# Performance work log

Measured on AMD Instinct MI355X. Metric: run time of the kernel, lower is better.

The kernel has to match this reference:

```python
import jax, jax.numpy as jnp
import numpy as np

N_Q = 8
DIM = 128
CODEBOOK_SIZE = 1024


def setup_inputs() -> dict:
    key = jax.random.key(0)
    k1, k2 = jax.random.split(key)
    x = jax.random.normal(k1, (8, DIM, 4096), dtype=jnp.float32)
    codebooks = jax.random.normal(k2, (N_Q, CODEBOOK_SIZE, DIM), dtype=jnp.float32)
    return {"x": x, "codebooks": codebooks, "frame_rate": 75}


def _rvq(xt, codebooks):
    # xt: (B, T, D); codebooks: (n_q, K, D)
    def stage(carry, cb):
        residual, qout = carry
        # squared euclidean distance (B, T, K); argmin == Encodec's argmax of -dist
        d = (jnp.sum(residual * residual, axis=-1, keepdims=True)
             - 2.0 * jnp.einsum('btd,kd->btk', residual, cb)
             + jnp.sum(cb * cb, axis=-1))
        idx = jnp.argmin(d, axis=-1)                     # (B, T)
        q = cb[idx]                                       # gather: (B, T, D)
        # commit loss: mse(quantize.detach(), input)
        commit = jnp.mean((jax.lax.stop_gradient(q) - residual) ** 2)
        # straight-through estimator
        q_st = residual + jax.lax.stop_gradient(q - residual)
        return (residual - q_st, qout + q_st), (idx, commit)

    init = (xt, jnp.zeros_like(xt))
    (_, qout), (codes, commits) = jax.lax.scan(stage, init, codebooks)
    return qout, codes, commits


def reference(x, codebooks, frame_rate):
    # x: (B, D, T) -> (B, T, D)
    xt = jnp.swapaxes(x, 1, 2)
    qout, codes, commits = _rvq(xt, codebooks)
    quantized = jnp.swapaxes(qout, 1, 2)                 # (B, D, T)
    n_q, K, _ = codebooks.shape
    bw_per_q = np.log2(K) * frame_rate
    bw = jnp.asarray(n_q * bw_per_q, dtype=jnp.float32)
    penalty = jnp.mean(commits)
    return quantized, codes, bw, penalty
```

## Files before the change

kernel.cpp:

```cpp
#include <hip/hip_runtime.h>
#include <math.h>

#define Bsz 8
#define Dd  128
#define Tt  4096
#define Kk  1024
#define NQ  8
#define BT  (Bsz*Tt)
#define MT  128
#define NTHR 512
#define WV  8
#define DELTA 0.05f

typedef float f32x4 __attribute__((ext_vector_type(4)));
typedef short short8 __attribute__((ext_vector_type(8)));

__device__ __forceinline__ unsigned short f2bf(float x) {
    unsigned u = __float_as_uint(x);
    u += 0x7FFF + ((u >> 16) & 1);
    return (unsigned short)(u >> 16);
}
__device__ __forceinline__ float bf2f(unsigned short h) {
    return __uint_as_float(((unsigned)h) << 16);
}

__global__ void k_init(const float* __restrict__ x,
                       float* __restrict__ resid) {
    __shared__ float tile[32][33];
    int b  = blockIdx.z;
    int t0 = blockIdx.x * 32, d0 = blockIdx.y * 32;
    int tx = threadIdx.x, ty = threadIdx.y;
    #pragma unroll
    for (int k = 0; k < 4; k++) {
        int d = d0 + ty + k * 8;
        tile[ty + k * 8][tx] = x[((size_t)(b * Dd + d)) * Tt + t0 + tx];
    }
    __syncthreads();
    #pragma unroll
    for (int k = 0; k < 4; k++) {
        int t = t0 + ty + k * 8;
        resid[((size_t)(b * Tt + t)) * Dd + d0 + tx] = tile[tx][ty + k * 8];
    }
}

__global__ void k_prep(const float* __restrict__ cb, char* __restrict__ bswz) {
    int ln = threadIdx.x;
    int kc = blockIdx.x & 3;
    int t  = (blockIdx.x >> 2) & 63;
    int q  = blockIdx.x >> 8;
    int code = t * 16 + (ln & 15);
    int d0   = kc * 32 + (ln >> 4) * 8;
    const float* src = cb + ((size_t)(q * Kk + code)) * Dd + d0;
    float v[8];
    *(float4*)&v[0] = *(const float4*)src;
    *(float4*)&v[4] = *(const float4*)(src + 4);
    short8 h, l;
    #pragma unroll
    for (int j = 0; j < 8; j++) {
        unsigned short hu = f2bf(v[j]);
        h[j] = (short)hu;
        l[j] = (short)f2bf(v[j] - bf2f(hu));
    }
    char* base = bswz + ((size_t)(q * 64 + t)) * 8192;
    *(short8*)(base + kc * 1024 + ln * 16) = h;
    *(short8*)(base + 4096 + kc * 1024 + ln * 16) = l;
}

__global__ void k_c2(const float* __restrict__ cb,
                     float* __restrict__ c2,
                     double* __restrict__ commits) {
    int row  = blockIdx.x * 4 + (threadIdx.x >> 6);
    int lane = threadIdx.x & 63;
    const float* p = cb + (size_t)row * Dd;
    float a = p[lane], b = p[lane + 64];
    float s = a * a + b * b;
    #pragma unroll
    for (int off = 32; off; off >>= 1) s += __shfl_down(s, off);
    if (lane == 0) c2[row] = s;
    if (blockIdx.x == 0 && threadIdx.x < NQ) commits[threadIdx.x] = 0.0;
}

__device__ __forceinline__ float exact_score(const float* __restrict__ rrow,
                                             const float* __restrict__ crow,
                                             float c2v) {
    float a = 0.0f;
    #pragma unroll
    for (int d4 = 0; d4 < 32; d4++) {
        float4 r = *(const float4*)(rrow + d4 * 4);
        float4 c = *(const float4*)(crow + d4 * 4);
        a = fmaf(r.x, c.x, a); a = fmaf(r.y, c.y, a);
        a = fmaf(r.z, c.z, a); a = fmaf(r.w, c.w, a);
    }
    return fmaf(-2.0f, a, c2v);
}

__global__ __launch_bounds__(NTHR, 2) void k_rvq_fused(
        float* __restrict__ resid,
        const float* __restrict__ cb,
        const char*  __restrict__ bswz,
        const float* __restrict__ c2g,
        float* __restrict__ codes_f,
        double* __restrict__ commits) {
    __shared__ float rlds[MT][Dd];
    __shared__ float c2s[Kk];
    __shared__ f32x4 bbuf[2][NTHR];
    __shared__ float fb1[MT], fb2[MT], fb3[MT];
    __shared__ int   fi1[MT], fi2[MT];
    __shared__ int   sidxs[MT];
    __shared__ int   nfall, flist[MT];
    __shared__ float fwv[WV]; __shared__ int fwi[WV];
    __shared__ float csum[WV];

    const int tid  = threadIdx.x;
    const int w    = tid >> 6, ln = tid & 63;
    const int quad = ln >> 4,  m  = ln & 15;
    const int base = blockIdx.x * MT;
    const int prow = w * 16 + m;

    {
        const f32x4* src = (const f32x4*)(resid + (size_t)base * Dd);
        f32x4* dst = (f32x4*)&rlds[0][0];
        #pragma unroll
        for (int i = 0; i < (MT * Dd / 4) / NTHR; i++)
            dst[tid + i * NTHR] = src[tid + i * NTHR];
    }
    bbuf[0][tid] = *((const f32x4*)bswz + tid);
    int par = 0;
    __syncthreads();

    #pragma unroll 1
    for (int q = 0; q < NQ; q++) {
        const float* cbq = cb + (size_t)q * Kk * Dd;
        #pragma unroll
        for (int i = 0; i < Kk / NTHR; i++)
            c2s[tid + i * NTHR] = c2g[q * Kk + tid + i * NTHR];
        if (tid == 0) nfall = 0;

        short8 Ah[4], Al[4];
        #pragma unroll
        for (int kc = 0; kc < 4; kc++) {
            const float* rp = &rlds[prow][kc * 32 + quad * 8];
            float v[8];
            *(f32x4*)&v[0] = *(const f32x4*)rp;
            *(f32x4*)&v[4] = *(const f32x4*)(rp + 4);
            short8 h, l;
            #pragma unroll
            for (int j = 0; j < 8; j++) {
                unsigned short hu = f2bf(v[j]);
                h[j] = (short)hu;
                l[j] = (short)f2bf(v[j] - bf2f(hu));
            }
            Ah[kc] = h; Al[kc] = l;
        }

        float b1[4], b2[4], b3[4]; int i1[4], i2[4];
        #pragma unroll
        for (int j = 0; j < 4; j++) {
            b1[j] = INFINITY; b2[j] = INFINITY; b3[j] = INFINITY;
            i1[j] = 0; i2[j] = 0;
        }
        __syncthreads();

        #pragma unroll 2
        for (int t = 0; t < 64; t++) {
            const int tt = q * 64 + t;
            const bool havestg = (tt + 1 < NQ * 64);
            f32x4 stg;
            if (havestg)
                stg = *((const f32x4*)(bswz + (size_t)(tt + 1) * 8192) + tid);

            const char* bb = (const char*)&bbuf[par][0];
            f32x4 acc01 = {0.f, 0.f, 0.f, 0.f};
            f32x4 acc23 = {0.f, 0.f, 0.f, 0.f};
            #pragma unroll
            for (int kc = 0; kc < 4; kc++) {
                short8 ch = *(const short8*)(bb + kc * 1024 + ln * 16);
                short8 cl = *(const short8*)(bb + 4096 + kc * 1024 + ln * 16);
                if (kc < 2) {
                    acc01 = __builtin_amdgcn_mfma_f32_16x16x32_bf16(Al[kc], ch, acc01, 0, 0, 0);
                    acc01 = __builtin_amdgcn_mfma_f32_16x16x32_bf16(Ah[kc], cl, acc01, 0, 0, 0);
                    acc01 = __builtin_amdgcn_mfma_f32_16x16x32_bf16(Ah[kc], ch, acc01, 0, 0, 0);
                } else {
                    acc23 = __builtin_amdgcn_mfma_f32_16x16x32_bf16(Al[kc], ch, acc23, 0, 0, 0);
                    acc23 = __builtin_amdgcn_mfma_f32_16x16x32_bf16(Ah[kc], cl, acc23, 0, 0, 0);
                    acc23 = __builtin_amdgcn_mfma_f32_16x16x32_bf16(Ah[kc], ch, acc23, 0, 0, 0);
                }
            }
            float c2v  = c2s[t * 16 + m];
            int   code = t * 16 + m;
            #pragma unroll
            for (int j = 0; j < 4; j++) {
                float s = fmaf(-2.0f, acc01[j] + acc23[j], c2v);
                bool lt1 = s < b1[j];
                bool lt2 = s < b2[j];
                b3[j] = __builtin_amdgcn_fmed3f(s, b2[j], b3[j]);
                b2[j] = __builtin_amdgcn_fmed3f(s, b1[j], b2[j]);
                i2[j] = lt1 ? i1[j] : (lt2 ? code : i2[j]);
                i1[j] = lt1 ? code : i1[j];
                b1[j] = fminf(b1[j], s);
            }
            if (havestg) bbuf[par ^ 1][tid] = stg;
            __syncthreads();
            par ^= 1;
        }

        #pragma unroll
        for (int j = 0; j < 4; j++) {
            float v1 = b1[j], v2 = b2[j], v3 = b3[j];
            int   a1 = i1[j], a2 = i2[j];
            #pragma unroll
            for (int off = 1; off < 16; off <<= 1) {
                float w1 = __shfl_xor(v1, off); int j1 = __shfl_xor(a1, off);
                float w2 = __shfl_xor(v2, off); int j2 = __shfl_xor(a2, off);
                float w3 = __shfl_xor(v3, off);
                bool aw = (v1 < w1) || (v1 == w1 && a1 < j1);
                float x1 = aw ? v1 : w1, x2 = aw ? v2 : w2, x3 = aw ? v3 : w3;
                int   y1 = aw ? a1 : j1, y2 = aw ? a2 : j2;
                float z1 = aw ? w1 : v1, z2 = aw ? w2 : v2;
                int   u1 = aw ? j1 : a1;
                bool s2a = (x2 < z1) || (x2 == z1 && y2 < u1);
                v1 = x1; a1 = y1;
                v2 = s2a ? x2 : z1; a2 = s2a ? y2 : u1;
                v3 = s2a ? fminf(x3, z1) : fminf(x2, z2);
            }
            if (m == 0) {
                int p = w * 16 + quad * 4 + j;
                fb1[p] = v1; fb2[p] = v2; fb3[p] = v3;
                fi1[p] = a1; fi2[p] = a2;
            }
        }
        __syncthreads();

        if (tid < MT) {
            int p = tid;
            float v1 = fb1[p], v2 = fb2[p], v3 = fb3[p];
            int   a1 = fi1[p], a2 = fi2[p];
            if (v3 <= v1 + DELTA) {
                int sl = atomicAdd(&nfall, 1);
                flist[sl] = p;
            } else {
                int bk = a1;
                if (v2 <= v1 + DELTA) {
                    const float* rrow = &rlds[p][0];
                    float s1 = exact_score(rrow, cbq + (size_t)a1 * Dd, c2s[a1]);
                    float s2 = exact_score(rrow, cbq + (size_t)a2 * Dd, c2s[a2]);
                    if (s2 < s1 || (s2 == s1 && a2 < a1)) bk = a2;
                }
                sidxs[p] = bk;
                codes_f[(size_t)q * BT + base + p] = (float)bk;
            }
        }
        __syncthreads();

        for (int fi = 0; fi < nfall; fi++) {
            int p = flist[fi];
            const float* rrow = &rlds[p][0];
            float bv = INFINITY; int bk = 0;
            #pragma unroll
            for (int c = 0; c < 2; c++) {
                int k = tid * 2 + c;
                float sc = exact_score(rrow, cbq + (size_t)k * Dd, c2s[k]);
                if (sc < bv || (sc == bv && k < bk)) { bv = sc; bk = k; }
            }
            #pragma unroll
            for (int off = 32; off; off >>= 1) {
                float v2 = __shfl_xor(bv, off);
                int   k2 = __shfl_xor(bk, off);
                if (v2 < bv || (v2 == bv && k2 < bk)) { bv = v2; bk = k2; }
            }
            if (ln == 0) { fwv[w] = bv; fwi[w] = bk; }
            __syncthreads();
            if (tid == 0) {
                float v = fwv[0]; int k = fwi[0];
                #pragma unroll
                for (int w2 = 1; w2 < WV; w2++) {
                    if (fwv[w2] < v || (fwv[w2] == v && fwi[w2] < k)) {
                        v = fwv[w2]; k = fwi[w2];
                    }
                }
                sidxs[p] = k;
                codes_f[(size_t)q * BT + base + p] = (float)k;
            }
            __syncthreads();
        }
        __syncthreads();

        {
            const int idx = sidxs[prow];
            const float* qrow = cbq + (size_t)idx * Dd;
            float cacc = 0.0f;
            #pragma unroll
            for (int kc = 0; kc < 4; kc++) {
                const int d0 = kc * 32 + quad * 8;
                float r[8], qv[8], nr[8];
                *(f32x4*)&r[0]  = *(const f32x4*)&rlds[prow][d0];
                *(f32x4*)&r[4]  = *(const f32x4*)&rlds[prow][d0 + 4];
                *(f32x4*)&qv[0] = *(const f32x4*)(qrow + d0);
                *(f32x4*)&qv[4] = *(const f32x4*)(qrow + d0 + 4);
                #pragma unroll
                for (int j = 0; j < 8; j++) {
                    float t1 = qv[j] - r[j];
                    float qs = r[j] + t1;
                    nr[j] = r[j] - qs;
                    cacc = fmaf(t1, t1, cacc);
                }
                *(f32x4*)&rlds[prow][d0]     = *(f32x4*)&nr[0];
                *(f32x4*)&rlds[prow][d0 + 4] = *(f32x4*)&nr[4];
            }
            #pragma unroll
            for (int off = 32; off; off >>= 1) cacc += __shfl_down(cacc, off);
            if (ln == 0) csum[w] = cacc;
        }
        __syncthreads();
        if (tid == 0) {
            double sd = 0.0;
            #pragma unroll
            for (int w2 = 0; w2 < WV; w2++) sd += (double)csum[w2];
            atomicAdd(commits + q, sd);
        }
        __syncthreads();
    }

    {
        f32x4* dst = (f32x4*)(resid + (size_t)base * Dd);
        const f32x4* src = (const f32x4*)&rlds[0][0];
        #pragma unroll
        for (int i = 0; i < (MT * Dd / 4) / NTHR; i++)
            dst[tid + i * NTHR] = src[tid + i * NTHR];
    }
}

__global__ void k_final(const float* __restrict__ x,
                        const float* __restrict__ resid,
                        float* __restrict__ outq) {
    __shared__ float tile[32][33];
    int b  = blockIdx.z;
    int t0 = blockIdx.x * 32, d0 = blockIdx.y * 32;
    int tx = threadIdx.x, ty = threadIdx.y;
    #pragma unroll
    for (int k = 0; k < 4; k++) {
        int t = t0 + ty + k * 8;
        tile[ty + k * 8][tx] = resid[((size_t)(b * Tt + t)) * Dd + d0 + tx];
    }
    __syncthreads();
    #pragma unroll
    for (int k = 0; k < 4; k++) {
        int d = d0 + ty + k * 8;
        size_t o = ((size_t)(b * Dd + d)) * Tt + t0 + tx;
        outq[o] = x[o] - tile[tx][ty + k * 8];
    }
}

__global__ void k_scalars(const double* __restrict__ commits,
                          const int* __restrict__ frame_rate,
                          float* __restrict__ outs) {
    if (threadIdx.x == 0 && blockIdx.x == 0) {
        double s = 0.0;
        #pragma unroll
        for (int q = 0; q < NQ; q++) s += commits[q];
        double per_elem = s / ((double)NQ * (double)BT * (double)Dd);
        outs[0] = (float)(NQ * 10.0 * (double)frame_rate[0]);
        outs[1] = (float)per_elem;
    }
}

extern "C" void kernel_launch(void* const* d_in, const int* in_sizes, int n_in,
                              void* d_out, int out_size, void* d_ws, size_t ws_size,
                              hipStream_t stream) {
    const float* x  = (const float*)d_in[0];
    const float* cb = (const float*)d_in[1];
    const int*   fr = (const int*)d_in[2];

    float* outq    = (float*)d_out;
    float* codes_f = outq + (size_t)Bsz * Dd * Tt;
    float* scal    = codes_f + (size_t)NQ * BT;

    char* ws = (char*)d_ws;
    float*  resid   = (float*)ws;
    float*  c2      = resid + (size_t)BT * Dd;
    double* commits = (double*)(c2 + (size_t)NQ * Kk);
    char*   bswz    = (char*)(commits + NQ);

    dim3 tb(32, 8, 1);
    k_init<<<dim3(Tt / 32, Dd / 32, Bsz), tb, 0, stream>>>(x, resid);
    k_prep<<<NQ * 256, 64, 0, stream>>>(cb, bswz);
    k_c2<<<NQ * Kk / 4, 256, 0, stream>>>(cb, c2, commits);

    k_rvq_fused<<<BT / MT, NTHR, 0, stream>>>(resid, cb, bswz, c2,
                                              codes_f, commits);

    k_final<<<dim3(Tt / 32, Dd / 32, Bsz), tb, 0, stream>>>(x, resid, outq);
    k_scalars<<<1, 64, 0, stream>>>(commits, fr, scal);
}
```

Baseline: 507.6 us.

## Split codebook across wave halves, two row tiles per wave, async LDS loads

Each wave now holds two 16-row A fragments and processes half of the codebook tiles, so every B fragment read from LDS feeds twice as many MFMAs. The two halves' top-3 candidates are merged afterwards. Codebook tiles are streamed straight into LDS with global_load_lds using explicit waitcnt and barriers in place of register staging. The residual tile in LDS is XOR-swizzled to avoid bank conflicts, and MFMA sections run at raised priority. The cost is more registers per thread (which may limit occupancy at 2 blocks per CU), an extra merge step, and more complex synchronisation.

```diff
diff --git a/kernel.cpp b/kernel.cpp
--- a/kernel.cpp
+++ b/kernel.cpp
@@ -22,6 +22,12 @@
 }
 __device__ __forceinline__ float bf2f(unsigned short h) {
     return __uint_as_float(((unsigned)h) << 16);
+}
+
+__device__ __forceinline__ void gload_lds16(const void* g, void* l) {
+    __builtin_amdgcn_global_load_lds(
+        (const __attribute__((address_space(1))) unsigned int*)g,
+        (__attribute__((address_space(3))) unsigned int*)l, 16, 0, 0);
 }
 
 __global__ void k_init(const float* __restrict__ x,
@@ -80,16 +86,20 @@
     if (blockIdx.x == 0 && threadIdx.x < NQ) commits[threadIdx.x] = 0.0;
 }
 
-__device__ __forceinline__ float exact_score(const float* __restrict__ rrow,
-                                             const float* __restrict__ crow,
-                                             float c2v) {
+__device__ __forceinline__ float exact_score_sw(const float* __restrict__ rldsb,
+                                                int p,
+                                                const float* __restrict__ crow,
+                                                float c2v) {
+    const f32x4* r4 = (const f32x4*)rldsb;
+    const f32x4* c4 = (const f32x4*)crow;
+    int rb = p * 32, sw = p & 7;
     float a = 0.0f;
     #pragma unroll
     for (int d4 = 0; d4 < 32; d4++) {
-        float4 r = *(const float4*)(rrow + d4 * 4);
-        float4 c = *(const float4*)(crow + d4 * 4);
-        a = fmaf(r.x, c.x, a); a = fmaf(r.y, c.y, a);
-        a = fmaf(r.z, c.z, a); a = fmaf(r.w, c.w, a);
+        f32x4 r = r4[rb + (d4 ^ sw)];
+        f32x4 c = c4[d4];
+        a = fmaf(r[0], c[0], a); a = fmaf(r[1], c[1], a);
+        a = fmaf(r[2], c[2], a); a = fmaf(r[3], c[3], a);
     }
     return fmaf(-2.0f, a, c2v);
 }
@@ -101,11 +111,12 @@
         const float* __restrict__ c2g,
         float* __restrict__ codes_f,
         double* __restrict__ commits) {
-    __shared__ float rlds[MT][Dd];
+    __shared__ float rlds[MT * Dd];
     __shared__ float c2s[Kk];
-    __shared__ f32x4 bbuf[2][NTHR];
-    __shared__ float fb1[MT], fb2[MT], fb3[MT];
-    __shared__ int   fi1[MT], fi2[MT];
+    __shared__ f32x4 bbuf[2][2][512];
+    __shared__ float fA1[MT], fA2[MT], fA3[MT];
+    __shared__ float fB1[MT], fB2[MT], fB3[MT];
+    __shared__ int   iA1[MT], iA2[MT], iB1[MT], iB2[MT];
     __shared__ int   sidxs[MT];
     __shared__ int   nfall, flist[MT];
     __shared__ float fwv[WV]; __shared__ int fwi[WV];
@@ -114,136 +125,201 @@
     const int tid  = threadIdx.x;
     const int w    = tid >> 6, ln = tid & 63;
     const int quad = ln >> 4,  m  = ln & 15;
+    const int wg   = w & 3,    half = w >> 2;
+    const int toff = half * 32;
     const int base = blockIdx.x * MT;
-    const int prow = w * 16 + m;
+    const int prow0 = wg * 32 + m;
+    const int prow1 = wg * 32 + 16 + m;
+
+    f32x4* r4 = (f32x4*)rlds;
 
     {
         const f32x4* src = (const f32x4*)(resid + (size_t)base * Dd);
-        f32x4* dst = (f32x4*)&rlds[0][0];
-        #pragma unroll
-        for (int i = 0; i < (MT * Dd / 4) / NTHR; i++)
-            dst[tid + i * NTHR] = src[tid + i * NTHR];
-    }
-    bbuf[0][tid] = *((const f32x4*)bswz + tid);
-    int par = 0;
+        #pragma unroll
+        for (int i = 0; i < (MT * Dd / 4) / NTHR; i++) {
+            int idx = tid + i * NTHR;
+            int row = idx >> 5, c4 = idx & 31;
+            r4[row * 32 + (c4 ^ (row & 7))] = src[idx];
+        }
+    }
     __syncthreads();
 
     #pragma unroll 1
     for (int q = 0; q < NQ; q++) {
         const float* cbq = cb + (size_t)q * Kk * Dd;
+        const char*  bsq = bswz + (size_t)q * 64 * 8192;
         #pragma unroll
         for (int i = 0; i < Kk / NTHR; i++)
             c2s[tid + i * NTHR] = c2g[q * Kk + tid + i * NTHR];
         if (tid == 0) nfall = 0;
 
-        short8 Ah[4], Al[4];
+        short8 Ah0[4], Al0[4], Ah1[4], Al1[4];
         #pragma unroll
         for (int kc = 0; kc < 4; kc++) {
-            const float* rp = &rlds[prow][kc * 32 + quad * 8];
+            int c4a = kc * 8 + quad * 2;
             float v[8];
-            *(f32x4*)&v[0] = *(const f32x4*)rp;
-            *(f32x4*)&v[4] = *(const f32x4*)(rp + 4);
             short8 h, l;
+            *(f32x4*)&v[0] = r4[prow0 * 32 + (c4a ^ (prow0 & 7))];
+            *(f32x4*)&v[4] = r4[prow0 * 32 + ((c4a + 1) ^ (prow0 & 7))];
             #pragma unroll
             for (int j = 0; j < 8; j++) {
                 unsigned short hu = f2bf(v[j]);
                 h[j] = (short)hu;
                 l[j] = (short)f2bf(v[j] - bf2f(hu));
             }
-            Ah[kc] = h; Al[kc] = l;
-        }
-
-        float b1[4], b2[4], b3[4]; int i1[4], i2[4];
+            Ah0[kc] = h; Al0[kc] = l;
+            *(f32x4*)&v[0] = r4[prow1 * 32 + (c4a ^ (prow1 & 7))];
+            *(f32x4*)&v[4] = r4[prow1 * 32 + ((c4a + 1) ^ (prow1 & 7))];
+            #pragma unroll
+            for (int j = 0; j < 8; j++) {
+                unsigned short hu = f2bf(v[j]);
+                h[j] = (short)hu;
+                l[j] = (short)f2bf(v[j] - bf2f(hu));
+            }
+            Ah1[kc] = h; Al1[kc] = l;
+        }
+
+        float b1a[4], b2a[4], b3a[4], b1b[4], b2b[4], b3b[4];
+        int   i1a[4], i2a[4], i1b[4], i2b[4];
         #pragma unroll
         for (int j = 0; j < 4; j++) {
-            b1[j] = INFINITY; b2[j] = INFINITY; b3[j] = INFINITY;
-            i1[j] = 0; i2[j] = 0;
-        }
-        __syncthreads();
-
-        #pragma unroll 2
-        for (int t = 0; t < 64; t++) {
-            const int tt = q * 64 + t;
-            const bool havestg = (tt + 1 < NQ * 64);
-            f32x4 stg;
-            if (havestg)
-                stg = *((const f32x4*)(bswz + (size_t)(tt + 1) * 8192) + tid);
-
-            const char* bb = (const char*)&bbuf[par][0];
-            f32x4 acc01 = {0.f, 0.f, 0.f, 0.f};
-            f32x4 acc23 = {0.f, 0.f, 0.f, 0.f};
+            b1a[j] = INFINITY; b2a[j] = INFINITY; b3a[j] = INFINITY;
+            b1b[j] = INFINITY; b2b[j] = INFINITY; b3b[j] = INFINITY;
+            i1a[j] = 0; i2a[j] = 0; i1b[j] = 0; i2b[j] = 0;
+        }
+        __syncthreads();
+
+        gload_lds16(bsq + (size_t)toff * 0 + 0 * 8192 + w * 1024 + ln * 16,
+                    (char*)&bbuf[0][0][0] + w * 1024);
+        gload_lds16(bsq + (size_t)32 * 8192 + w * 1024 + ln * 16,
+                    (char*)&bbuf[0][1][0] + w * 1024);
+        int par = 0;
+
+        #pragma unroll 1
+        for (int s = 0; s < 32; s++) {
+            asm volatile("s_waitcnt vmcnt(0)" ::: "memory");
+            __builtin_amdgcn_s_barrier();
+            __builtin_amdgcn_sched_barrier(0);
+            if (s + 1 < 32) {
+                gload_lds16(bsq + (size_t)(s + 1) * 8192 + w * 1024 + ln * 16,
+                            (char*)&bbuf[par ^ 1][0][0] + w * 1024);
+                gload_lds16(bsq + (size_t)(32 + s + 1) * 8192 + w * 1024 + ln * 16,
+                            (char*)&bbuf[par ^ 1][1][0] + w * 1024);
+            }
+            const char* bb = (const char*)&bbuf[par][half][0];
+            f32x4 a01a = {0.f,0.f,0.f,0.f}, a23a = {0.f,0.f,0.f,0.f};
+            f32x4 a01b = {0.f,0.f,0.f,0.f}, a23b = {0.f,0.f,0.f,0.f};
+            __builtin_amdgcn_s_setprio(1);
             #pragma unroll
             for (int kc = 0; kc < 4; kc++) {
                 short8 ch = *(const short8*)(bb + kc * 1024 + ln * 16);
                 short8 cl = *(const short8*)(bb + 4096 + kc * 1024 + ln * 16);
                 if (kc < 2) {
-                    acc01 = __builtin_amdgcn_mfma_f32_16x16x32_bf16(Al[kc], ch, acc01, 0, 0, 0);
-                    acc01 = __builtin_amdgcn_mfma_f32_16x16x32_bf16(Ah[kc], cl, acc01, 0, 0, 0);
-                    acc01 = __builtin_amdgcn_mfma_f32_16x16x32_bf16(Ah[kc], ch, acc01, 0, 0, 0);
+                    a01a = __builtin_amdgcn_mfma_f32_16x16x32_bf16(Al0[kc], ch, a01a, 0, 0, 0);
+                    a01a = __builtin_amdgcn_mfma_f32_16x16x32_bf16(Ah0[kc], cl, a01a, 0, 0, 0);
+                    a01a = __builtin_amdgcn_mfma_f32_16x16x32_bf16(Ah0[kc], ch, a01a, 0, 0, 0);
+                    a01b = __builtin_amdgcn_mfma_f32_16x16x32_bf16(Al1[kc], ch, a01b, 0, 0, 0);
+                    a01b = __builtin_amdgcn_mfma_f32_16x16x32_bf16(Ah1[kc], cl, a01b, 0, 0, 0);
+                    a01b = __builtin_amdgcn_mfma_f32_16x16x32_bf16(Ah1[kc], ch, a01b, 0, 0, 0);
                 } else {
-                    acc23 = __builtin_amdgcn_mfma_f32_16x16x32_bf16(Al[kc], ch, acc23, 0, 0, 0);
-                    acc23 = __builtin_amdgcn_mfma_f32_16x16x32_bf16(Ah[kc], cl, acc23, 0, 0, 0);
-                    acc23 = __builtin_amdgcn_mfma_f32_16x16x32_bf16(Ah[kc], ch, acc23, 0, 0, 0);
+                    a23a = __builtin_amdgcn_mfma_f32_16x16x32_bf16(Al0[kc], ch, a23a, 0, 0, 0);
+                    a23a = __builtin_amdgcn_mfma_f32_16x16x32_bf16(Ah0[kc], cl, a23a, 0, 0, 0);
+                    a23a = __builtin_amdgcn_mfma_f32_16x16x32_bf16(Ah0[kc], ch, a23a, 0, 0, 0);
+                    a23b = __builtin_amdgcn_mfma_f32_16x16x32_bf16(Al1[kc], ch, a23b, 0, 0, 0);
+                    a23b = __builtin_amdgcn_mfma_f32_16x16x32_bf16(Ah1[kc], cl, a23b, 0, 0, 0);
+                    a23b = __builtin_amdgcn_mfma_f32_16x16x32_bf16(Ah1[kc], ch, a23b, 0, 0, 0);
                 }
             }
-            float c2v  = c2s[t * 16 + m];
-            int   code = t * 16 + m;
+            __builtin_amdgcn_s_setprio(0);
+            float c2v  = c2s[(toff + s) * 16 + m];
+            int   code = (toff + s) * 16 + m;
             #pragma unroll
             for (int j = 0; j < 4; j++) {
-                float s = fmaf(-2.0f, acc01[j] + acc23[j], c2v);
-                bool lt1 = s < b1[j];
-                bool lt2 = s < b2[j];
-                b3[j] = __builtin_amdgcn_fmed3f(s, b2[j], b3[j]);
-                b2[j] = __builtin_amdgcn_fmed3f(s, b1[j], b2[j]);
-                i2[j] = lt1 ? i1[j] : (lt2 ? code : i2[j]);
-                i1[j] = lt1 ? code : i1[j];
-                b1[j] = fminf(b1[j], s);
-            }
-            if (havestg) bbuf[par ^ 1][tid] = stg;
-            __syncthreads();
+                float sc = fmaf(-2.0f, a01a[j] + a23a[j], c2v);
+                bool lt1 = sc < b1a[j];
+                bool lt2 = sc < b2a[j];
+                b3a[j] = __builtin_amdgcn_fmed3f(sc, b2a[j], b3a[j]);
+                b2a[j] = __builtin_amdgcn_fmed3f(sc, b1a[j], b2a[j]);
+                i2a[j] = lt1 ? i1a[j] : (lt2 ? code : i2a[j]);
+                i1a[j] = lt1 ? code : i1a[j];
+                b1a[j] = fminf(b1a[j], sc);
+                float sd = fmaf(-2.0f, a01b[j] + a23b[j], c2v);
+                bool mt1 = sd < b1b[j];
+                bool mt2 = sd < b2b[j];
+                b3b[j] = __builtin_amdgcn_fmed3f(sd, b2b[j], b3b[j]);
+                b2b[j] = __builtin_amdgcn_fmed3f(sd, b1b[j], b2b[j]);
+                i2b[j] = mt1 ? i1b[j] : (mt2 ? code : i2b[j]);
+                i1b[j] = mt1 ? code : i1b[j];
+                b1b[j] = fminf(b1b[j], sd);
+            }
+            asm volatile("s_waitcnt lgkmcnt(0)" ::: "memory");
+            __builtin_amdgcn_sched_barrier(0);
             par ^= 1;
         }
 
         #pragma unroll
-        for (int j = 0; j < 4; j++) {
-            float v1 = b1[j], v2 = b2[j], v3 = b3[j];
-            int   a1 = i1[j], a2 = i2[j];
-            #pragma unroll
-            for (int off = 1; off < 16; off <<= 1) {
-                float w1 = __shfl_xor(v1, off); int j1 = __shfl_xor(a1, off);
-                float w2 = __shfl_xor(v2, off); int j2 = __shfl_xor(a2, off);
-                float w3 = __shfl_xor(v3, off);
-                bool aw = (v1 < w1) || (v1 == w1 && a1 < j1);
-                float x1 = aw ? v1 : w1, x2 = aw ? v2 : w2, x3 = aw ? v3 : w3;
-                int   y1 = aw ? a1 : j1, y2 = aw ? a2 : j2;
-                float z1 = aw ? w1 : v1, z2 = aw ? w2 : v2;
-                int   u1 = aw ? j1 : a1;
-                bool s2a = (x2 < z1) || (x2 == z1 && y2 < u1);
-                v1 = x1; a1 = y1;
-                v2 = s2a ? x2 : z1; a2 = s2a ? y2 : u1;
-                v3 = s2a ? fminf(x3, z1) : fminf(x2, z2);
-            }
-            if (m == 0) {
-                int p = w * 16 + quad * 4 + j;
-                fb1[p] = v1; fb2[p] = v2; fb3[p] = v3;
-                fi1[p] = a1; fi2[p] = a2;
+        for (int set = 0; set < 2; set++) {
+            #pragma unroll
+            for (int j = 0; j < 4; j++) {
+                float v1 = set ? b1b[j] : b1a[j];
+                float v2 = set ? b2b[j] : b2a[j];
+                float v3 = set ? b3b[j] : b3a[j];
+                int   a1 = set ? i1b[j] : i1a[j];
+                int   a2 = set ? i2b[j] : i2a[j];
+                #pragma unroll
+                for (int off = 1; off < 16; off <<= 1) {
+                    float w1 = __shfl_xor(v1, off); int j1 = __shfl_xor(a1, off);
+                    float w2 = __shfl_xor(v2, off); int j2 = __shfl_xor(a2, off);
+                    float w3 = __shfl_xor(v3, off);
+                    bool aw = (v1 < w1) || (v1 == w1 && a1 < j1);
+                    float x1 = aw ? v1 : w1, x2 = aw ? v2 : w2, x3 = aw ? v3 : w3;
+                    int   y1 = aw ? a1 : j1, y2 = aw ? a2 : j2;
+                    float z1 = aw ? w1 : v1, z2 = aw ? w2 : v2;
+                    int   u1 = aw ? j1 : a1;
+                    bool s2a = (x2 < z1) || (x2 == z1 && y2 < u1);
+                    v1 = x1; a1 = y1;
+                    v2 = s2a ? x2 : z1; a2 = s2a ? y2 : u1;
+                    v3 = s2a ? fminf(x3, z1) : fminf(x2, z2);
+                }
+                if (m == 0) {
+                    int p = wg * 32 + set * 16 + quad * 4 + j;
+                    if (half == 0) {
+                        fA1[p] = v1; fA2[p] = v2; fA3[p] = v3;
+                        iA1[p] = a1; iA2[p] = a2;
+                    } else {
+                        fB1[p] = v1; fB2[p] = v2; fB3[p] = v3;
+                        iB1[p] = a1; iB2[p] = a2;
+                    }
+                }
             }
         }
         __syncthreads();
 
         if (tid < MT) {
             int p = tid;
-            float v1 = fb1[p], v2 = fb2[p], v3 = fb3[p];
-            int   a1 = fi1[p], a2 = fi2[p];
+            float vA1 = fA1[p], vA2 = fA2[p], vA3 = fA3[p];
+            int   aA1 = iA1[p], aA2 = iA2[p];
+            float vB1 = fB1[p], vB2 = fB2[p], vB3 = fB3[p];
+            int   aB1 = iB1[p], aB2 = iB2[p];
+            bool aw = (vA1 < vB1) || (vA1 == vB1 && aA1 < aB1);
+            float x1 = aw ? vA1 : vB1, x2 = aw ? vA2 : vB2, x3 = aw ? vA3 : vB3;
+            int   y1 = aw ? aA1 : aB1, y2 = aw ? aA2 : aB2;
+            float z1 = aw ? vB1 : vA1, z2 = aw ? vB2 : vA2;
+            int   u1 = aw ? aB1 : aA1;
+            bool s2a = (x2 < z1) || (x2 == z1 && y2 < u1);
+            float v1 = x1;
+            float v2 = s2a ? x2 : z1;
+            float v3 = s2a ? fminf(x3, z1) : fminf(x2, z2);
+            int   a1 = y1;
+            int   a2 = s2a ? y2 : u1;
             if (v3 <= v1 + DELTA) {
                 int sl = atomicAdd(&nfall, 1);
                 flist[sl] = p;
             } else {
                 int bk = a1;
                 if (v2 <= v1 + DELTA) {
-                    const float* rrow = &rlds[p][0];
-                    float s1 = exact_score(rrow, cbq + (size_t)a1 * Dd, c2s[a1]);
-                    float s2 = exact_score(rrow, cbq + (size_t)a2 * Dd, c2s[a2]);
+                    float s1 = exact_score_sw(rlds, p, cbq + (size_t)a1 * Dd, c2s[a1]);
+                    float s2 = exact_score_sw(rlds, p, cbq + (size_t)a2 * Dd, c2s[a2]);
                     if (s2 < s1 || (s2 == s1 && a2 < a1)) bk = a2;
                 }
                 sidxs[p] = bk;
@@ -254,12 +330,11 @@
 
         for (int fi = 0; fi < nfall; fi++) {
             int p = flist[fi];
-            const float* rrow = &rlds[p][0];
             float bv = INFINITY; int bk = 0;
             #pragma unroll
             for (int c = 0; c < 2; c++) {
                 int k = tid * 2 + c;
-                float sc = exact_score(rrow, cbq + (size_t)k * Dd, c2s[k]);
+                float sc = exact_score_sw(rlds, p, cbq + (size_t)k * Dd, c2s[k]);
                 if (sc < bv || (sc == bv && k < bk)) { bv = sc; bk = k; }
             }
             #pragma unroll
@@ -286,26 +361,22 @@
         __syncthreads();
 
         {
-            const int idx = sidxs[prow];
-            const float* qrow = cbq + (size_t)idx * Dd;
+            int p = tid >> 2;
+            int rb = p * 32, sw = p & 7, cb4 = (tid & 3) * 8;
+            const float* qrow = cbq + ((size_t)sidxs[p]) * Dd + (tid & 3) * 32;
             float cacc = 0.0f;
             #pragma unroll
-            for (int kc = 0; kc < 4; kc++) {
-                const int d0 = kc * 32 + quad * 8;
-                float r[8], qv[8], nr[8];
-                *(f32x4*)&r[0]  = *(const f32x4*)&rlds[prow][d0];
-                *(f32x4*)&r[4]  = *(const f32x4*)&rlds[prow][d0 + 4];
-                *(f32x4*)&qv[0] = *(const f32x4*)(qrow + d0);
-                *(f32x4*)&qv[4] = *(const f32x4*)(qrow + d0 + 4);
-                #pragma unroll
-                for (int j = 0; j < 8; j++) {
-                    float t1 = qv[j] - r[j];
-                    float qs = r[j] + t1;
-                    nr[j] = r[j] - qs;
-                    cacc = fmaf(t1, t1, cacc);
-                }
-                *(f32x4*)&rlds[prow][d0]     = *(f32x4*)&nr[0];
-                *(f32x4*)&rlds[prow][d0 + 4] = *(f32x4*)&nr[4];
+            for (int hh = 0; hh < 8; hh++) {
+                f32x4 r  = r4[rb + ((cb4 + hh) ^ sw)];
+                f32x4 qv = *(const f32x4*)(qrow + hh * 4);
+                float t1x = qv[0] - r[0], t1y = qv[1] - r[1];
+                float t1z = qv[2] - r[2], t1w = qv[3] - r[3];
+                float qsx = r[0] + t1x, qsy = r[1] + t1y;
+                float qsz = r[2] + t1z, qsw = r[3] + t1w;
+                f32x4 nr = { r[0] - qsx, r[1] - qsy, r[2] - qsz, r[3] - qsw };
+                r4[rb + ((cb4 + hh) ^ sw)] = nr;
+                cacc = fmaf(t1x, t1x, cacc); cacc = fmaf(t1y, t1y, cacc);
+                cacc = fmaf(t1z, t1z, cacc); cacc = fmaf(t1w, t1w, cacc);
             }
             #pragma unroll
             for (int off = 32; off; off >>= 1) cacc += __shfl_down(cacc, off);
@@ -323,10 +394,12 @@
 
     {
         f32x4* dst = (f32x4*)(resid + (size_t)base * Dd);
-        const f32x4* src = (const f32x4*)&rlds[0][0];
-        #pragma unroll
-        for (int i = 0; i < (MT * Dd / 4) / NTHR; i++)
-            dst[tid + i * NTHR] = src[tid + i * NTHR];
+        #pragma unroll
+        for (int i = 0; i < (MT * Dd / 4) / NTHR; i++) {
+            int idx = tid + i * NTHR;
+            int row = idx >> 5, c4 = idx & 31;
+            dst[idx] = r4[row * 32 + (c4 ^ (row & 7))];
+        }
     }
 }
 
```

Result: slower. 560.7 us (+10.5%).

## Swizzle residual LDS layout and software-pipeline MFMA tiles with argmin scoring

Applied to the files above, without the earlier changes.

Stores the residual tile in LDS with an XOR swizzle on 16-byte chunks to avoid bank conflicts in the A-fragment loads, the exact rescoring and the residual update, and reorganises the residual update so each row is handled by four consecutive threads. The main codebook loop is restructured into even/odd tiles so the MFMAs for the next tile are issued before the top-3 scoring of the previous tile, with s_setprio raised around the MFMA block. This is meant to overlap matrix-core work with the VALU compare chain and cut LDS conflicts. In exchange it uses more registers for the second accumulator set, which may hurt occupancy at two blocks per CU.

```diff
diff --git a/kernel.cpp b/kernel.cpp
--- a/kernel.cpp
+++ b/kernel.cpp
@@ -80,16 +80,20 @@
     if (blockIdx.x == 0 && threadIdx.x < NQ) commits[threadIdx.x] = 0.0;
 }
 
-__device__ __forceinline__ float exact_score(const float* __restrict__ rrow,
-                                             const float* __restrict__ crow,
-                                             float c2v) {
+__device__ __forceinline__ float exact_score_sw(const float* __restrict__ rldsb,
+                                                int p,
+                                                const float* __restrict__ crow,
+                                                float c2v) {
+    const f32x4* r4 = (const f32x4*)rldsb;
+    const f32x4* c4 = (const f32x4*)crow;
+    int rb = p * 32, sw = p & 7;
     float a = 0.0f;
     #pragma unroll
     for (int d4 = 0; d4 < 32; d4++) {
-        float4 r = *(const float4*)(rrow + d4 * 4);
-        float4 c = *(const float4*)(crow + d4 * 4);
-        a = fmaf(r.x, c.x, a); a = fmaf(r.y, c.y, a);
-        a = fmaf(r.z, c.z, a); a = fmaf(r.w, c.w, a);
+        f32x4 r = r4[rb + (d4 ^ sw)];
+        f32x4 c = c4[d4];
+        a = fmaf(r[0], c[0], a); a = fmaf(r[1], c[1], a);
+        a = fmaf(r[2], c[2], a); a = fmaf(r[3], c[3], a);
     }
     return fmaf(-2.0f, a, c2v);
 }
@@ -101,9 +105,9 @@
         const float* __restrict__ c2g,
         float* __restrict__ codes_f,
         double* __restrict__ commits) {
-    __shared__ float rlds[MT][Dd];
+    __shared__ float rlds[MT * Dd];
     __shared__ float c2s[Kk];
-    __shared__ f32x4 bbuf[2][NTHR];
+    __shared__ f32x4 bbuf[2][512];
     __shared__ float fb1[MT], fb2[MT], fb3[MT];
     __shared__ int   fi1[MT], fi2[MT];
     __shared__ int   sidxs[MT];
@@ -117,12 +121,16 @@
     const int base = blockIdx.x * MT;
     const int prow = w * 16 + m;
 
+    f32x4* r4 = (f32x4*)rlds;
+
     {
         const f32x4* src = (const f32x4*)(resid + (size_t)base * Dd);
-        f32x4* dst = (f32x4*)&rlds[0][0];
-        #pragma unroll
-        for (int i = 0; i < (MT * Dd / 4) / NTHR; i++)
-            dst[tid + i * NTHR] = src[tid + i * NTHR];
+        #pragma unroll
+        for (int i = 0; i < (MT * Dd / 4) / NTHR; i++) {
+            int idx = tid + i * NTHR;
+            int row = idx >> 5, c4 = idx & 31;
+            r4[row * 32 + (c4 ^ (row & 7))] = src[idx];
+        }
     }
     bbuf[0][tid] = *((const f32x4*)bswz + tid);
     int par = 0;
@@ -139,10 +147,10 @@
         short8 Ah[4], Al[4];
         #pragma unroll
         for (int kc = 0; kc < 4; kc++) {
-            const float* rp = &rlds[prow][kc * 32 + quad * 8];
+            int c4a = kc * 8 + quad * 2;
             float v[8];
-            *(f32x4*)&v[0] = *(const f32x4*)rp;
-            *(f32x4*)&v[4] = *(const f32x4*)(rp + 4);
+            *(f32x4*)&v[0] = r4[prow * 32 + (c4a ^ (prow & 7))];
+            *(f32x4*)&v[4] = r4[prow * 32 + ((c4a + 1) ^ (prow & 7))];
             short8 h, l;
             #pragma unroll
             for (int j = 0; j < 8; j++) {
@@ -161,36 +169,33 @@
         }
         __syncthreads();
 
-        #pragma unroll 2
-        for (int t = 0; t < 64; t++) {
-            const int tt = q * 64 + t;
-            const bool havestg = (tt + 1 < NQ * 64);
-            f32x4 stg;
-            if (havestg)
-                stg = *((const f32x4*)(bswz + (size_t)(tt + 1) * 8192) + tid);
-
-            const char* bb = (const char*)&bbuf[par][0];
-            f32x4 acc01 = {0.f, 0.f, 0.f, 0.f};
-            f32x4 acc23 = {0.f, 0.f, 0.f, 0.f};
+        auto MFMA_TILE = [&](f32x4& A01, f32x4& A23) {
+            const short8* Bt = (const short8*)&bbuf[par][0];
+            A01 = (f32x4){0.f, 0.f, 0.f, 0.f};
+            A23 = (f32x4){0.f, 0.f, 0.f, 0.f};
+            __builtin_amdgcn_s_setprio(1);
             #pragma unroll
             for (int kc = 0; kc < 4; kc++) {
-                short8 ch = *(const short8*)(bb + kc * 1024 + ln * 16);
-                short8 cl = *(const short8*)(bb + 4096 + kc * 1024 + ln * 16);
+                short8 ch = Bt[kc * 64 + ln];
+                short8 cl = Bt[256 + kc * 64 + ln];
                 if (kc < 2) {
-                    acc01 = __builtin_amdgcn_mfma_f32_16x16x32_bf16(Al[kc], ch, acc01, 0, 0, 0);
-                    acc01 = __builtin_amdgcn_mfma_f32_16x16x32_bf16(Ah[kc], cl, acc01, 0, 0, 0);
-                    acc01 = __builtin_amdgcn_mfma_f32_16x16x32_bf16(Ah[kc], ch, acc01, 0, 0, 0);
+                    A01 = __builtin_amdgcn_mfma_f32_16x16x32_bf16(Al[kc], ch, A01, 0, 0, 0);
+                    A01 = __builtin_amdgcn_mfma_f32_16x16x32_bf16(Ah[kc], cl, A01, 0, 0, 0);
+                    A01 = __builtin_amdgcn_mfma_f32_16x16x32_bf16(Ah[kc], ch, A01, 0, 0, 0);
                 } else {
-                    acc23 = __builtin_amdgcn_mfma_f32_16x16x32_bf16(Al[kc], ch, acc23, 0, 0, 0);
-                    acc23 = __builtin_amdgcn_mfma_f32_16x16x32_bf16(Ah[kc], cl, acc23, 0, 0, 0);
-                    acc23 = __builtin_amdgcn_mfma_f32_16x16x32_bf16(Ah[kc], ch, acc23, 0, 0, 0);
+                    A23 = __builtin_amdgcn_mfma_f32_16x16x32_bf16(Al[kc], ch, A23, 0, 0, 0);
+                    A23 = __builtin_amdgcn_mfma_f32_16x16x32_bf16(Ah[kc], cl, A23, 0, 0, 0);
+                    A23 = __builtin_amdgcn_mfma_f32_16x16x32_bf16(Ah[kc], ch, A23, 0, 0, 0);
                 }
             }
-            float c2v  = c2s[t * 16 + m];
-            int   code = t * 16 + m;
+            __builtin_amdgcn_s_setprio(0);
+        };
+        auto SCORE = [&](const f32x4& A01, const f32x4& A23, int TT) {
+            float c2v  = c2s[TT * 16 + m];
+            int   code = TT * 16 + m;
             #pragma unroll
             for (int j = 0; j < 4; j++) {
-                float s = fmaf(-2.0f, acc01[j] + acc23[j], c2v);
+                float s = fmaf(-2.0f, A01[j] + A23[j], c2v);
                 bool lt1 = s < b1[j];
                 bool lt2 = s < b2[j];
                 b3[j] = __builtin_amdgcn_fmed3f(s, b2[j], b3[j]);
@@ -199,10 +204,33 @@
                 i1[j] = lt1 ? code : i1[j];
                 b1[j] = fminf(b1[j], s);
             }
-            if (havestg) bbuf[par ^ 1][tid] = stg;
+        };
+
+        f32x4 aE01, aE23, aO01, aO23;
+        #pragma unroll 1
+        for (int t2 = 0; t2 < 32; t2++) {
+            const int e   = 2 * t2;
+            const int tte = q * 64 + e;
+            f32x4 stg;
+            const bool hs1 = (tte + 1 < NQ * 64);
+            if (hs1)
+                stg = *((const f32x4*)(bswz + (size_t)(tte + 1) * 8192) + tid);
+            MFMA_TILE(aE01, aE23);
+            if (t2 > 0) SCORE(aO01, aO23, e - 1);
+            if (hs1) bbuf[par ^ 1][tid] = stg;
             __syncthreads();
             par ^= 1;
-        }
+            const int tto = tte + 1;
+            const bool hs2 = (tto + 1 < NQ * 64);
+            if (hs2)
+                stg = *((const f32x4*)(bswz + (size_t)(tto + 1) * 8192) + tid);
+            MFMA_TILE(aO01, aO23);
+            SCORE(aE01, aE23, e);
+            if (hs2) bbuf[par ^ 1][tid] = stg;
+            __syncthreads();
+            par ^= 1;
+        }
+        SCORE(aO01, aO23, 63);
 
         #pragma unroll
         for (int j = 0; j < 4; j++) {
@@ -241,9 +269,8 @@
             } else {
                 int bk = a1;
                 if (v2 <= v1 + DELTA) {
-                    const float* rrow = &rlds[p][0];
-                    float s1 = exact_score(rrow, cbq + (size_t)a1 * Dd, c2s[a1]);
-                    float s2 = exact_score(rrow, cbq + (size_t)a2 * Dd, c2s[a2]);
+                    float s1 = exact_score_sw(rlds, p, cbq + (size_t)a1 * Dd, c2s[a1]);
+                    float s2 = exact_score_sw(rlds, p, cbq + (size_t)a2 * Dd, c2s[a2]);
                     if (s2 < s1 || (s2 == s1 && a2 < a1)) bk = a2;
                 }
                 sidxs[p] = bk;
@@ -254,12 +281,11 @@
 
         for (int fi = 0; fi < nfall; fi++) {
             int p = flist[fi];
-            const float* rrow = &rlds[p][0];
             float bv = INFINITY; int bk = 0;
             #pragma unroll
             for (int c = 0; c < 2; c++) {
                 int k = tid * 2 + c;
-                float sc = exact_score(rrow, cbq + (size_t)k * Dd, c2s[k]);
+                float sc = exact_score_sw(rlds, p, cbq + (size_t)k * Dd, c2s[k]);
                 if (sc < bv || (sc == bv && k < bk)) { bv = sc; bk = k; }
             }
             #pragma unroll
@@ -286,26 +312,22 @@
         __syncthreads();
 
         {
-            const int idx = sidxs[prow];
-            const float* qrow = cbq + (size_t)idx * Dd;
+            int p = tid >> 2;
+            int rb = p * 32, sw = p & 7, cb4 = (tid & 3) * 8;
+            const float* qrow = cbq + ((size_t)sidxs[p]) * Dd + (tid & 3) * 32;
             float cacc = 0.0f;
             #pragma unroll
-            for (int kc = 0; kc < 4; kc++) {
-                const int d0 = kc * 32 + quad * 8;
-                float r[8], qv[8], nr[8];
-                *(f32x4*)&r[0]  = *(const f32x4*)&rlds[prow][d0];
-                *(f32x4*)&r[4]  = *(const f32x4*)&rlds[prow][d0 + 4];
-                *(f32x4*)&qv[0] = *(const f32x4*)(qrow + d0);
-                *(f32x4*)&qv[4] = *(const f32x4*)(qrow + d0 + 4);
-                #pragma unroll
-                for (int j = 0; j < 8; j++) {
-                    float t1 = qv[j] - r[j];
-                    float qs = r[j] + t1;
-                    nr[j] = r[j] - qs;
-                    cacc = fmaf(t1, t1, cacc);
-                }
-                *(f32x4*)&rlds[prow][d0]     = *(f32x4*)&nr[0];
-                *(f32x4*)&rlds[prow][d0 + 4] = *(f32x4*)&nr[4];
+            for (int hh = 0; hh < 8; hh++) {
+                f32x4 r  = r4[rb + ((cb4 + hh) ^ sw)];
+                f32x4 qv = *(const f32x4*)(qrow + hh * 4);
+                float t1x = qv[0] - r[0], t1y = qv[1] - r[1];
+                float t1z = qv[2] - r[2], t1w = qv[3] - r[3];
+                float qsx = r[0] + t1x, qsy = r[1] + t1y;
+                float qsz = r[2] + t1z, qsw = r[3] + t1w;
+                f32x4 nr = { r[0] - qsx, r[1] - qsy, r[2] - qsz, r[3] - qsw };
+                r4[rb + ((cb4 + hh) ^ sw)] = nr;
+                cacc = fmaf(t1x, t1x, cacc); cacc = fmaf(t1y, t1y, cacc);
+                cacc = fmaf(t1z, t1z, cacc); cacc = fmaf(t1w, t1w, cacc);
             }
             #pragma unroll
             for (int off = 32; off; off >>= 1) cacc += __shfl_down(cacc, off);
@@ -323,10 +345,12 @@
 
     {
         f32x4* dst = (f32x4*)(resid + (size_t)base * Dd);
-        const f32x4* src = (const f32x4*)&rlds[0][0];
-        #pragma unroll
-        for (int i = 0; i < (MT * Dd / 4) / NTHR; i++)
-            dst[tid + i * NTHR] = src[tid + i * NTHR];
+        #pragma unroll
+        for (int i = 0; i < (MT * Dd / 4) / NTHR; i++) {
+            int idx = tid + i * NTHR;
+            int row = idx >> 5, c4 = idx & 31;
+            dst[idx] = r4[row * 32 + (c4 ^ (row & 7))];
+        }
     }
 }
 
```

New measurement: 788.4 us. 55.3% more time.
